# Performance work log

Hardware: AMD Instinct MI355X
Metric: run time of the kernel (lower is better)

The kernel has to match this reference:

```python
import jax, jax.numpy as jnp
import numpy as np

B, T, HID, H, DH, K = 2, 1024, 1024, 16, 64, 4
ROPE_BASE = 10000.0
EPS = 1e-6


def _causal_dwconv(x, w, b):
    # x: (B, T, C); w: (C, 1, K) depthwise; causal left-pad K-1, then SiLU
    xc = jnp.transpose(x, (0, 2, 1))  # (B, C, T)
    y = jax.lax.conv_general_dilated(
        xc, w, window_strides=(1,), padding=[(K - 1, 0)],
        dimension_numbers=('NCH', 'OIH', 'NCH'), feature_group_count=xc.shape[1])
    y = y + b[None, :, None]
    return jax.nn.silu(jnp.transpose(y, (0, 2, 1)))


def _rope(x, cos, sin):
    # x: (B, T, H, D); cos/sin: (T, D) with emb = cat(freqs, freqs)
    c = cos[None, :, None, :]
    s = sin[None, :, None, :]
    x1, x2 = x[..., ::2], x[..., 1::2]
    return jnp.concatenate(
        [x1 * c[..., ::2] - x2 * s[..., ::2],
         x1 * s[..., ::2] + x2 * c[..., ::2]], axis=-1)


def _delta_rule(q, k, v, alpha, beta, D_param):
    # q,k,v: (B,T,H,DH); alpha,beta: (B,T,H)
    # S_t = alpha_t * (I - beta_t k_t k_t^T) S_{t-1} + beta_t k_t v_t^T
    # o_t  = q_t^T S_t-1-style readout + D * (q.k) * v   (matches torch einsum 'bhd,bhde->bhe')
    qs = jnp.moveaxis(q, 1, 0).astype(jnp.float32)  # (T,B,H,DH)
    ks = jnp.moveaxis(k, 1, 0).astype(jnp.float32)
    vs = jnp.moveaxis(v, 1, 0).astype(jnp.float32)
    als = jnp.moveaxis(alpha, 1, 0).astype(jnp.float32)  # (T,B,H)
    bes = jnp.moveaxis(beta, 1, 0).astype(jnp.float32)

    def step(S, inp):
        qt, kt, vt, at, bt = inp
        ot = jnp.einsum('bhd,bhde->bhe', qt, S)
        ot = ot + D_param[None, :, None] * jnp.sum(qt * kt, -1, keepdims=True) * vt
        kS = jnp.einsum('bhd,bhde->bhe', kt, S)  # k^T S
        at_ = at[..., None, None]
        bt_ = bt[..., None, None]
        S_new = at_ * (S - bt_ * kt[..., :, None] * kS[..., None, :]) \
                + bt_ * kt[..., :, None] * vt[..., None, :]
        return S_new, ot

    S0 = jnp.zeros((q.shape[0], H, DH, DH), jnp.float32)
    _, outs = jax.lax.scan(step, S0, (qs, ks, vs, als, bes))
    return jnp.moveaxis(outs, 0, 1)  # (B,T,H,DH)


def _forward(x, Wq, Wk, Wv, Wg, Wo, bw, bb, gkw, gkb,
             qcw, qcb, kcw, kcb, vcw, vcb, A_log, D_param, dt_bias, onorm_w):
    Bb, Tt, _ = x.shape
    q = _causal_dwconv(x @ Wq, qcw, qcb).reshape(Bb, Tt, H, DH)
    k = _causal_dwconv(x @ Wk, kcw, kcb).reshape(Bb, Tt, H, DH)
    v = _causal_dwconv(x @ Wv, vcw, vcb).reshape(Bb, Tt, H, DH)

    # RoPE (computed on the fly, fp32)
    t = jnp.arange(Tt, dtype=jnp.float32)
    inv_freq = 1.0 / (ROPE_BASE ** (jnp.arange(0, DH, 2, dtype=jnp.float32) / DH))
    freqs = jnp.outer(t, inv_freq)
    emb = jnp.concatenate([freqs, freqs], -1)
    cos, sin = jnp.cos(emb), jnp.sin(emb)
    q = _rope(q, cos, sin)
    k = _rope(k, cos, sin)

    # L2-normalize q/k (delta-net stability, NOT softmax)
    q = q * jax.lax.rsqrt(jnp.sum(q * q, -1, keepdims=True) + EPS)
    k = k * jax.lax.rsqrt(jnp.sum(k * k, -1, keepdims=True) + EPS)

    beta = jax.nn.sigmoid(x @ bw + bb)  # (B,T,H) writing strength
    alpha = jnp.exp(-jnp.exp(A_log) * jax.nn.softplus(x @ gkw + gkb + dt_bias))  # (B,T,H) decay

    o = _delta_rule(q, k, v, alpha, beta, D_param)  # (B,T,H,DH)

    # gated RMSNorm output: g * silu(RMSNorm(o))
    g = (x @ Wg).reshape(Bb, Tt, H, DH)
    on = o * jax.lax.rsqrt(jnp.mean(o * o, -1, keepdims=True) + EPS) * onorm_w
    o = g * jax.nn.silu(on)
    return o.reshape(Bb, Tt, H * DH) @ Wo


def setup_inputs() -> dict:
    key = jax.random.key(0)
    ks = jax.random.split(key, 20)
    w = lambda i, shape, s=0.02: (jax.random.normal(ks[i], shape, jnp.float32) * s)
    return {
        'x': jax.random.normal(ks[0], (B, T, HID), jnp.float32),
        'Wq': w(1, (HID, H * DH)), 'Wk': w(2, (HID, H * DH)),
        'Wv': w(3, (HID, H * DH)), 'Wg': w(4, (HID, H * DH)),
        'Wo': w(5, (H * DH, HID)),
        'bw': w(6, (HID, H)), 'bb': jnp.zeros((H,), jnp.float32),
        'gkw': w(7, (HID, H)), 'gkb': jnp.zeros((H,), jnp.float32),
        'qcw': w(8, (H * DH, 1, K), 0.3), 'qcb': jnp.zeros((H * DH,), jnp.float32),
        'kcw': w(9, (H * DH, 1, K), 0.3), 'kcb': jnp.zeros((H * DH,), jnp.float32),
        'vcw': w(10, (H * DH, 1, K), 0.3), 'vcb': jnp.zeros((H * DH,), jnp.float32),
        'A_log': jnp.log(jax.random.uniform(ks[11], (H,), jnp.float32, 1.0, 16.0)),
        'D_param': jnp.ones((H,), jnp.float32),
        'dt_bias': jax.random.uniform(ks[12], (H,), jnp.float32, -0.01, 0.01),
        'onorm_w': jnp.ones((DH,), jnp.float32),
    }


def reference(x, Wq, Wk, Wv, Wg, Wo, bw, bb, gkw, gkb,
              qcw, qcb, kcw, kcb, vcw, vcb, A_log, D_param, dt_bias, onorm_w):
    return _forward(x, Wq, Wk, Wv, Wg, Wo, bw, bb, gkw, gkb,
                    qcw, qcb, kcw, kcb, vcw, vcb, A_log, D_param, dt_bias, onorm_w)
```

## Files before the change

### kernel.cpp

```cpp
#include <hip/hip_runtime.h>
#include <hip/hip_bf16.h>
#include <cstdint>

#define T_LEN 1024
#define HIDN  1024
#define NH    16
#define DHD   64

typedef __bf16 bf16x8 __attribute__((ext_vector_type(8)));
typedef float  f32x4  __attribute__((ext_vector_type(4)));

__device__ inline void split8(float4 x0, float4 x1, uint4& hi, uint4& lo) {
  union { __bf16 h[8]; uint4 u; } ph, pl;
  float v[8] = {x0.x, x0.y, x0.z, x0.w, x1.x, x1.y, x1.z, x1.w};
#pragma unroll
  for (int j = 0; j < 8; j++) {
    __bf16 h = (__bf16)v[j];
    ph.h[j] = h;
    pl.h[j] = (__bf16)(v[j] - (float)h);
  }
  hi = ph.u; lo = pl.u;
}

__global__ __launch_bounds__(256) void k_transp_split(
    const float* __restrict__ W0, const float* __restrict__ W1,
    const float* __restrict__ W2, const float* __restrict__ W3,
    const float* __restrict__ W4,
    __bf16* __restrict__ H0, __bf16* __restrict__ H1, __bf16* __restrict__ H2,
    __bf16* __restrict__ H3, __bf16* __restrict__ H4,
    __bf16* __restrict__ L0, __bf16* __restrict__ L1, __bf16* __restrict__ L2,
    __bf16* __restrict__ L3, __bf16* __restrict__ L4) {
  const float* W; __bf16* Th; __bf16* Tl;
  switch (blockIdx.z) {
    case 0: W = W0; Th = H0; Tl = L0; break;
    case 1: W = W1; Th = H1; Tl = L1; break;
    case 2: W = W2; Th = H2; Tl = L2; break;
    case 3: W = W3; Th = H3; Tl = L3; break;
    default: W = W4; Th = H4; Tl = L4; break;
  }
  __shared__ float tile[64][65];
  int tid = threadIdx.x;
  int r0 = tid >> 4;
  int c0 = (tid & 15) * 4;
  int kbase = blockIdx.y * 64, nbase = blockIdx.x * 64;
#pragma unroll
  for (int rr = 0; rr < 4; rr++) {
    int r = r0 + rr * 16;
    float4 v = *(const float4*)(W + (size_t)(kbase + r) * 1024 + nbase + c0);
    tile[r][c0 + 0] = v.x; tile[r][c0 + 1] = v.y;
    tile[r][c0 + 2] = v.z; tile[r][c0 + 3] = v.w;
  }
  __syncthreads();
#pragma unroll
  for (int rr = 0; rr < 4; rr++) {
    int n = r0 + rr * 16;
    union { __bf16 h[4]; unsigned long long u; } ph, pl;
#pragma unroll
    for (int j = 0; j < 4; j++) {
      float v = tile[c0 + j][n];
      __bf16 h = (__bf16)v;
      ph.h[j] = h;
      pl.h[j] = (__bf16)(v - (float)h);
    }
    *(unsigned long long*)(Th + (size_t)(nbase + n) * 1024 + kbase + c0) = ph.u;
    *(unsigned long long*)(Tl + (size_t)(nbase + n) * 1024 + kbase + c0) = pl.u;
  }
}

#define LDT 40
__global__ __launch_bounds__(256) void k_gemm3f(
    const float* __restrict__ Af,
    const __bf16* __restrict__ Bh0, const __bf16* __restrict__ Bh1,
    const __bf16* __restrict__ Bh2, const __bf16* __restrict__ Bh3,
    const __bf16* __restrict__ Bl0, const __bf16* __restrict__ Bl1,
    const __bf16* __restrict__ Bl2, const __bf16* __restrict__ Bl3,
    float* __restrict__ C0, float* __restrict__ C1,
    float* __restrict__ C2, float* __restrict__ C3,
    int Kdim, int Ncols) {
  const __bf16* Bh; const __bf16* Bl; float* C;
  switch (blockIdx.z) {
    case 0: Bh = Bh0; Bl = Bl0; C = C0; break;
    case 1: Bh = Bh1; Bl = Bl1; C = C1; break;
    case 2: Bh = Bh2; Bl = Bl2; C = C2; break;
    default: Bh = Bh3; Bl = Bl3; C = C3; break;
  }
  __shared__ __bf16 Ash[128 * LDT];
  __shared__ __bf16 Asl[128 * LDT];
  __shared__ __bf16 Bsh[128 * LDT];
  __shared__ __bf16 Bsl[128 * LDT];
  const int tid = threadIdx.x;
  const int lane = tid & 63;
  const int wave = tid >> 6;
  const int wr = wave >> 1, wc = wave & 1;
  const int rowA0 = blockIdx.y * 128;
  const int colB0 = blockIdx.x * 128;
  const int sseg = tid & 3;
  const int srow0 = tid >> 2;
  const int srow1 = srow0 + 64;

  f32x4 acc[4][4] = {};

  for (int k0 = 0; k0 < Kdim; k0 += 32) {
    size_t a0 = (size_t)(rowA0 + srow0) * Kdim + k0 + sseg * 8;
    size_t a1 = (size_t)(rowA0 + srow1) * Kdim + k0 + sseg * 8;
    size_t b0 = (size_t)(colB0 + srow0) * Kdim + k0 + sseg * 8;
    size_t b1 = (size_t)(colB0 + srow1) * Kdim + k0 + sseg * 8;
    float4 a00 = *(const float4*)(Af + a0);
    float4 a01 = *(const float4*)(Af + a0 + 4);
    float4 a10 = *(const float4*)(Af + a1);
    float4 a11 = *(const float4*)(Af + a1 + 4);
    uint4 rbh0 = *(const uint4*)(Bh + b0);
    uint4 rbh1 = *(const uint4*)(Bh + b1);
    uint4 rbl0 = *(const uint4*)(Bl + b0);
    uint4 rbl1 = *(const uint4*)(Bl + b1);
    uint4 rah0, ral0, rah1, ral1;
    split8(a00, a01, rah0, ral0);
    split8(a10, a11, rah1, ral1);
    __syncthreads();
    *(uint4*)&Ash[srow0 * LDT + sseg * 8] = rah0;
    *(uint4*)&Ash[srow1 * LDT + sseg * 8] = rah1;
    *(uint4*)&Asl[srow0 * LDT + sseg * 8] = ral0;
    *(uint4*)&Asl[srow1 * LDT + sseg * 8] = ral1;
    *(uint4*)&Bsh[srow0 * LDT + sseg * 8] = rbh0;
    *(uint4*)&Bsh[srow1 * LDT + sseg * 8] = rbh1;
    *(uint4*)&Bsl[srow0 * LDT + sseg * 8] = rbl0;
    *(uint4*)&Bsl[srow1 * LDT + sseg * 8] = rbl1;
    __syncthreads();
    bf16x8 afh[4], afl[4], bfh[4], bfl[4];
#pragma unroll
    for (int mi = 0; mi < 4; mi++) {
      int off = (wr * 64 + mi * 16 + (lane & 15)) * LDT + (lane >> 4) * 8;
      afh[mi] = *(const bf16x8*)&Ash[off];
      afl[mi] = *(const bf16x8*)&Asl[off];
    }
#pragma unroll
    for (int ni = 0; ni < 4; ni++) {
      int off = (wc * 64 + ni * 16 + (lane & 15)) * LDT + (lane >> 4) * 8;
      bfh[ni] = *(const bf16x8*)&Bsh[off];
      bfl[ni] = *(const bf16x8*)&Bsl[off];
    }
#pragma unroll
    for (int mi = 0; mi < 4; mi++)
#pragma unroll
      for (int ni = 0; ni < 4; ni++) {
        acc[mi][ni] = __builtin_amdgcn_mfma_f32_16x16x32_bf16(afh[mi], bfh[ni], acc[mi][ni], 0, 0, 0);
        acc[mi][ni] = __builtin_amdgcn_mfma_f32_16x16x32_bf16(afl[mi], bfh[ni], acc[mi][ni], 0, 0, 0);
        acc[mi][ni] = __builtin_amdgcn_mfma_f32_16x16x32_bf16(afh[mi], bfl[ni], acc[mi][ni], 0, 0, 0);
      }
  }
#pragma unroll
  for (int mi = 0; mi < 4; mi++)
#pragma unroll
    for (int ni = 0; ni < 4; ni++) {
      int col = colB0 + wc * 64 + ni * 16 + (lane & 15);
#pragma unroll
      for (int r = 0; r < 4; r++) {
        int row = rowA0 + wr * 64 + mi * 16 + (lane >> 4) * 4 + r;
        C[(size_t)row * Ncols + col] = acc[mi][ni][r];
      }
    }
}

__global__ __launch_bounds__(256) void k_gates(
    const float* __restrict__ x, const float* __restrict__ bw,
    const float* __restrict__ bb, const float* __restrict__ gkw,
    const float* __restrict__ gkb, const float* __restrict__ A_log,
    const float* __restrict__ dt_bias,
    float* __restrict__ alphaB, float* __restrict__ betaB) {
  const int bt = blockIdx.x;
  const int tid = threadIdx.x;
  const int h = tid & 15;
  const int chunk = tid >> 4;
  const float* xr = x + (size_t)bt * HIDN;
  float d1 = 0.f, d2 = 0.f;
#pragma unroll 8
  for (int j = 0; j < 64; j++) {
    int k = chunk * 64 + j;
    float xv = xr[k];
    d1 += xv * bw[k * 16 + h];
    d2 += xv * gkw[k * 16 + h];
  }
  __shared__ float p1[16][16], p2[16][16];
  p1[chunk][h] = d1; p2[chunk][h] = d2;
  __syncthreads();
  if (tid < 16) {
    float s1 = 0.f, s2 = 0.f;
#pragma unroll
    for (int c = 0; c < 16; c++) { s1 += p1[c][tid]; s2 += p2[c][tid]; }
    float beta = 1.f / (1.f + expf(-(s1 + bb[tid])));
    float z = s2 + gkb[tid] + dt_bias[tid];
    float sp = fmaxf(z, 0.f) + log1pf(expf(-fabsf(z)));
    float alpha = expf(-expf(A_log[tid]) * sp);
    alphaB[(size_t)bt * 16 + tid] = alpha;
    betaB[(size_t)bt * 16 + tid] = beta;
  }
}

__global__ __launch_bounds__(256) void k_cra(
    const float* __restrict__ qp, const float* __restrict__ kp,
    const float* __restrict__ vp,
    const float* __restrict__ qcw, const float* __restrict__ qcb,
    const float* __restrict__ kcw, const float* __restrict__ kcb,
    const float* __restrict__ vcw, const float* __restrict__ vcb,
    const float* __restrict__ alphaB, const float* __restrict__ betaB,
    const float* __restrict__ Dp,
    float* __restrict__ qr, float* __restrict__ kr, float* __restrict__ vr,
    float4* __restrict__ aux) {
  int widx = blockIdx.x * 4 + (threadIdx.x >> 6);
  int lane = threadIdx.x & 63;
  int h = widx & 15;
  int bt = widx >> 4;
  int t = bt & 1023, b = bt >> 10;
  int c = h * 64 + lane;
  size_t colbase = ((size_t)b * 1024) * 1024 + c;

  float4 wq = *(const float4*)(qcw + (size_t)c * 4);
  float4 wk = *(const float4*)(kcw + (size_t)c * 4);
  float4 wv = *(const float4*)(vcw + (size_t)c * 4);
  float aq = qcb[c], ak = kcb[c], av = vcb[c];
  {
    float x0 = qp[colbase + (size_t)t * 1024];
    float y0 = kp[colbase + (size_t)t * 1024];
    float z0 = vp[colbase + (size_t)t * 1024];
    aq += wq.w * x0; ak += wk.w * y0; av += wv.w * z0;
    if (t >= 1) {
      float x1 = qp[colbase + (size_t)(t - 1) * 1024];
      float y1 = kp[colbase + (size_t)(t - 1) * 1024];
      float z1 = vp[colbase + (size_t)(t - 1) * 1024];
      aq += wq.z * x1; ak += wk.z * y1; av += wv.z * z1;
    }
    if (t >= 2) {
      float x2 = qp[colbase + (size_t)(t - 2) * 1024];
      float y2 = kp[colbase + (size_t)(t - 2) * 1024];
      float z2v = vp[colbase + (size_t)(t - 2) * 1024];
      aq += wq.y * x2; ak += wk.y * y2; av += wv.y * z2v;
    }
    if (t >= 3) {
      float x3 = qp[colbase + (size_t)(t - 3) * 1024];
      float y3 = kp[colbase + (size_t)(t - 3) * 1024];
      float z3 = vp[colbase + (size_t)(t - 3) * 1024];
      aq += wq.x * x3; ak += wk.x * y3; av += wv.x * z3;
    }
  }
  float yq = aq / (1.f + expf(-aq));
  float yk = ak / (1.f + expf(-ak));
  float yv = av / (1.f + expf(-av));

  int i = lane & 31;
  float fr = expf(-(float)(2 * (i & 15)) * (9.210340371976184f / 32.f));
  float ang = (float)t * fr;
  float cv = cosf(ang), sv = sinf(ang);
  float q1 = __shfl(yq, 2 * i), q2 = __shfl(yq, 2 * i + 1);
  float k1 = __shfl(yk, 2 * i), k2 = __shfl(yk, 2 * i + 1);
  float qo = (lane < 32) ? (q1 * cv - q2 * sv) : (q1 * sv + q2 * cv);
  float ko = (lane < 32) ? (k1 * cv - k2 * sv) : (k1 * sv + k2 * cv);

  float qs = qo * qo, ks2 = ko * ko;
#pragma unroll
  for (int m = 1; m < 64; m <<= 1) { qs += __shfl_xor(qs, m); ks2 += __shfl_xor(ks2, m); }
  float qn = qo * rsqrtf(qs + 1e-6f);
  float kn = ko * rsqrtf(ks2 + 1e-6f);
  float dq = qn * kn;
#pragma unroll
  for (int m = 1; m < 64; m <<= 1) dq += __shfl_xor(dq, m);
  size_t obase = ((size_t)(b * 16 + h) * 1024 + t) * 64;
  qr[obase + lane] = qn;
  kr[obase + lane] = kn;
  vr[obase + lane] = yv;
  if (lane == 0) {
    float alpha = alphaB[(size_t)bt * 16 + h];
    float beta = betaB[(size_t)bt * 16 + h];
    aux[(size_t)(b * 16 + h) * 1024 + t] = make_float4(alpha, beta, alpha * beta, Dp[h] * dq);
  }
}

__global__ __launch_bounds__(256) void k_scanA(
    const float* __restrict__ qr, const float* __restrict__ kr,
    const float* __restrict__ vr, const float4* __restrict__ aux,
    float* __restrict__ O1, float* __restrict__ AcF,
    float* __restrict__ BcTF, float* __restrict__ QeffF,
    float* __restrict__ gcF) {
  const int bid = blockIdx.x;
  const int bh = bid >> 4, c = bid & 15;
  const int t0 = c * 64;
  const int tid = threadIdx.x;
  const int w = tid >> 6, lane = tid & 63;
  const float* qB = qr + (size_t)bh * 65536 + (size_t)t0 * 64;
  const float* kB = kr + (size_t)bh * 65536 + (size_t)t0 * 64;
  const float* vB = vr + (size_t)bh * 65536 + (size_t)t0 * 64;
  const float4* auxB = aux + (size_t)bh * T_LEN + t0;

  __shared__ __bf16 q_b[64 * 72];
  __shared__ __bf16 k_b[64 * 72];
  __shared__ __bf16 kT_b[64 * 72];
  __shared__ __bf16 C_b[64 * 72];
  __shared__ __bf16 U0T[64 * 72];
  __shared__ __bf16 WT[64 * 72];
  __shared__ float  vS[64 * 64];
  __shared__ float  MTf[64 * 68];
  __shared__ float  lgS[64], pvS[64], beS[64], awS[64], enS[64];

  if (w == 0) {
    float4 a4 = auxB[lane];
    float lg = logf(a4.x);
#pragma unroll
    for (int off = 1; off < 64; off <<= 1) {
      float tv = __shfl_up(lg, off);
      if (lane >= off) lg += tv;
    }
    float pv = __shfl_up(lg, 1);
    if (lane == 0) pv = 0.f;
    float lgTot = __shfl(lg, 63);
    lgS[lane] = lg; pvS[lane] = pv; beS[lane] = a4.y; awS[lane] = a4.w;
    enS[lane] = expf(lgTot - lg);
    if (lane == 0) gcF[bid] = expf(lgTot);
  }
#pragma unroll
  for (int p = 0; p < 2; p++) {
    int s = p * 256 + tid;
    int row = s >> 3, col8 = s & 7;
    const float* gq = qB + (size_t)row * 64 + col8 * 8;
    const float* gk = kB + (size_t)row * 64 + col8 * 8;
    const float* gv = vB + (size_t)row * 64 + col8 * 8;
    float4 q0 = *(const float4*)gq, q1 = *(const float4*)(gq + 4);
    float4 k0 = *(const float4*)gk, k1 = *(const float4*)(gk + 4);
    float4 v0 = *(const float4*)gv, v1 = *(const float4*)(gv + 4);
    union { __bf16 h[8]; uint4 u; } pq, pk;
    pq.h[0] = (__bf16)q0.x; pq.h[1] = (__bf16)q0.y; pq.h[2] = (__bf16)q0.z; pq.h[3] = (__bf16)q0.w;
    pq.h[4] = (__bf16)q1.x; pq.h[5] = (__bf16)q1.y; pq.h[6] = (__bf16)q1.z; pq.h[7] = (__bf16)q1.w;
    pk.h[0] = (__bf16)k0.x; pk.h[1] = (__bf16)k0.y; pk.h[2] = (__bf16)k0.z; pk.h[3] = (__bf16)k0.w;
    pk.h[4] = (__bf16)k1.x; pk.h[5] = (__bf16)k1.y; pk.h[6] = (__bf16)k1.z; pk.h[7] = (__bf16)k1.w;
    *(uint4*)&q_b[row * 72 + col8 * 8] = pq.u;
    *(uint4*)&k_b[row * 72 + col8 * 8] = pk.u;
    *(float4*)&vS[row * 64 + col8 * 8] = v0;
    *(float4*)&vS[row * 64 + col8 * 8 + 4] = v1;
  }
  __syncthreads();

  {
    const int mi = w;
#pragma unroll
    for (int ni = 0; ni < 4; ni++) {
      f32x4 akk = {0.f, 0.f, 0.f, 0.f};
      f32x4 aqk = {0.f, 0.f, 0.f, 0.f};
#pragma unroll
      for (int ks = 0; ks < 2; ks++) {
        bf16x8 fa_k = *(const bf16x8*)&k_b[(mi * 16 + (lane & 15)) * 72 + ks * 32 + (lane >> 4) * 8];
        bf16x8 fa_q = *(const bf16x8*)&q_b[(mi * 16 + (lane & 15)) * 72 + ks * 32 + (lane >> 4) * 8];
        bf16x8 fb_k = *(const bf16x8*)&k_b[(ni * 16 + (lane & 15)) * 72 + ks * 32 + (lane >> 4) * 8];
        akk = __builtin_amdgcn_mfma_f32_16x16x32_bf16(fa_k, fb_k, akk, 0, 0, 0);
        aqk = __builtin_amdgcn_mfma_f32_16x16x32_bf16(fa_q, fb_k, aqk, 0, 0, 0);
      }
#pragma unroll
      for (int r = 0; r < 4; r++) {
        int row = mi * 16 + (lane >> 4) * 4 + r;
        int col = ni * 16 + (lane & 15);
        float mt = 0.f, cv = 0.f;
        if (row > col) {
          mt = beS[row] * expf(lgS[row] - lgS[col]) * akk[r];
          cv = expf(pvS[row] - lgS[col]) * aqk[r];
        }
        MTf[col * 68 + row] = mt;
        C_b[row * 72 + col] = (__bf16)cv;
      }
    }
  }
  __syncthreads();

  if (w == 2) {
#pragma unroll
    for (int t8 = 0; t8 < 8; t8++) {
      union { __bf16 h[8]; uint4 u; } pt;
#pragma unroll
      for (int q = 0; q < 8; q++) {
        int t = t8 * 8 + q;
        pt.h[q] = (__bf16)((float)k_b[t * 72 + lane] * enS[t]);
      }
      *(uint4*)&kT_b[lane * 72 + t8 * 8] = pt.u;
    }
  }
  if (w < 2) {
    float u[64];
    if (w == 0) {
#pragma unroll
      for (int j = 0; j < 64; j++) u[j] = beS[j] * vS[j * 64 + lane];
    } else {
#pragma unroll
      for (int j = 0; j < 64; j++) u[j] = beS[j] * expf(lgS[j]) * (float)k_b[j * 72 + lane];
    }
    __bf16* dst = (w == 0) ? U0T : WT;
#pragma unroll
    for (int j = 0; j < 64; j++) {
      dst[lane * 72 + j] = (__bf16)u[j];
      float uj = u[j];
#pragma unroll
      for (int g = (j >> 4); g < 4; g++) {
#pragma unroll
        for (int q4 = 0; q4 < 4; q4++) {
          const float4 m4 = *(const float4*)&MTf[j * 68 + g * 16 + q4 * 4];
          u[g * 16 + q4 * 4 + 0] -= m4.x * uj;
          u[g * 16 + q4 * 4 + 1] -= m4.y * uj;
          u[g * 16 + q4 * 4 + 2] -= m4.z * uj;
          u[g * 16 + q4 * 4 + 3] -= m4.w * uj;
        }
      }
    }
  }
  __syncthreads();

  size_t cb = (size_t)bid * 4096;
  const int mi0 = (w >> 1) * 2;
  if ((w & 1) == 0) {
#pragma unroll
    for (int mm = 0; mm < 2; mm++) {
      int mi = mi0 + mm;
#pragma unroll
      for (int ni = 0; ni < 4; ni++) {
        f32x4 ab = {0.f, 0.f, 0.f, 0.f};
        f32x4 aa = {0.f, 0.f, 0.f, 0.f};
#pragma unroll
        for (int ks = 0; ks < 2; ks++) {
          int aoff = (mi * 16 + (lane & 15)) * 72 + ks * 32 + (lane >> 4) * 8;
          int boff = (ni * 16 + (lane & 15)) * 72 + ks * 32 + (lane >> 4) * 8;
          bf16x8 fu = *(const bf16x8*)&U0T[aoff];
          bf16x8 fkm = *(const bf16x8*)&kT_b[aoff];
          bf16x8 fkn = *(const bf16x8*)&kT_b[boff];
          bf16x8 fw = *(const bf16x8*)&WT[boff];
          ab = __builtin_amdgcn_mfma_f32_16x16x32_bf16(fu, fkn, ab, 0, 0, 0);
          aa = __builtin_amdgcn_mfma_f32_16x16x32_bf16(fkm, fw, aa, 0, 0, 0);
        }
#pragma unroll
        for (int r = 0; r < 4; r++) {
          int row = mi * 16 + (lane >> 4) * 4 + r;
          int col = ni * 16 + (lane & 15);
          BcTF[cb + row * 64 + col] = ab[r];
          AcF[cb + row * 64 + col] = aa[r];
        }
      }
    }
  } else {
#pragma unroll
    for (int mm = 0; mm < 2; mm++) {
      int mi = mi0 + mm;
#pragma unroll
      for (int ni = 0; ni < 4; ni++) {
        f32x4 ao = {0.f, 0.f, 0.f, 0.f};
        f32x4 ac = {0.f, 0.f, 0.f, 0.f};
#pragma unroll
        for (int ks = 0; ks < 2; ks++) {
          int aoff = (mi * 16 + (lane & 15)) * 72 + ks * 32 + (lane >> 4) * 8;
          int boff = (ni * 16 + (lane & 15)) * 72 + ks * 32 + (lane >> 4) * 8;
          bf16x8 fc = *(const bf16x8*)&C_b[aoff];
          bf16x8 fu = *(const bf16x8*)&U0T[boff];
          bf16x8 fw = *(const bf16x8*)&WT[boff];
          ao = __builtin_amdgcn_mfma_f32_16x16x32_bf16(fc, fu, ao, 0, 0, 0);
          ac = __builtin_amdgcn_mfma_f32_16x16x32_bf16(fc, fw, ac, 0, 0, 0);
        }
#pragma unroll
        for (int r = 0; r < 4; r++) {
          int t = mi * 16 + (lane >> 4) * 4 + r;
          int col = ni * 16 + (lane & 15);
          O1[(size_t)bh * 65536 + (size_t)(t0 + t) * 64 + col] =
              ao[r] + awS[t] * vS[t * 64 + col];
          QeffF[cb + t * 64 + col] = expf(pvS[t]) * (float)q_b[t * 72 + col] - ac[r];
        }
      }
    }
  }
}

__global__ __launch_bounds__(256) void k_scanB(
    const float* __restrict__ AcF, const float* __restrict__ BcTF,
    const float* __restrict__ gcF, float* __restrict__ S0TF) {
  const int bid = blockIdx.x;
  const int bh = bid >> 2, eg = bid & 3;
  const int e0 = eg * 16;
  const int tid = threadIdx.x;
  const int w = tid >> 6, lane = tid & 63;
  const int er = tid >> 2, seg = (tid & 3) * 16;
  const int er2 = tid >> 4, seg2 = (tid & 15) * 4;
  __shared__ float STf[16 * 68];
  __shared__ __bf16 Sh[16 * 72], Sl[16 * 72], Ac_b[64 * 72];
  *(float4*)&STf[er2 * 68 + seg2] = make_float4(0.f, 0.f, 0.f, 0.f);
  __syncthreads();

  size_t cbase = (size_t)bh * 16 * 4096;
  float4 acR[4];
  float bctR[4];
#pragma unroll
  for (int i = 0; i < 4; i++)
    acR[i] = *(const float4*)&AcF[cbase + er * 64 + seg + i * 4];
#pragma unroll
  for (int r = 0; r < 4; r++)
    bctR[r] = BcTF[cbase + (size_t)(e0 + (lane >> 4) * 4 + r) * 64 + w * 16 + (lane & 15)];

  for (int c = 0; c < 16; c++) {
    size_t cb = cbase + (size_t)c * 4096;
    {
      float4 s = *(const float4*)&STf[er2 * 68 + seg2];
      *(float4*)&S0TF[cb + (size_t)(e0 + er2) * 64 + seg2] = s;
      union { __bf16 h[4]; unsigned long long u; } ph, pl;
      float sv[4] = {s.x, s.y, s.z, s.w};
#pragma unroll
      for (int q = 0; q < 4; q++) {
        __bf16 hv = (__bf16)sv[q];
        ph.h[q] = hv;
        pl.h[q] = (__bf16)(sv[q] - (float)hv);
      }
      *(unsigned long long*)&Sh[er2 * 72 + seg2] = ph.u;
      *(unsigned long long*)&Sl[er2 * 72 + seg2] = pl.u;
    }
#pragma unroll
    for (int i = 0; i < 4; i++) {
      union { __bf16 h[4]; unsigned long long u; } pa;
      pa.h[0] = (__bf16)acR[i].x; pa.h[1] = (__bf16)acR[i].y;
      pa.h[2] = (__bf16)acR[i].z; pa.h[3] = (__bf16)acR[i].w;
      *(unsigned long long*)&Ac_b[er * 72 + seg + i * 4] = pa.u;
    }
    float gC = gcF[bh * 16 + c];
    __syncthreads();

    float4 acN[4];
    float bctN[4];
    if (c < 15) {
      size_t nb = cb + 4096;
#pragma unroll
      for (int i = 0; i < 4; i++)
        acN[i] = *(const float4*)&AcF[nb + er * 64 + seg + i * 4];
#pragma unroll
      for (int r = 0; r < 4; r++)
        bctN[r] = BcTF[nb + (size_t)(e0 + (lane >> 4) * 4 + r) * 64 + w * 16 + (lane & 15)];
    } else {
#pragma unroll
      for (int i = 0; i < 4; i++) acN[i] = acR[i];
#pragma unroll
      for (int r = 0; r < 4; r++) bctN[r] = bctR[r];
    }

    f32x4 acc = {0.f, 0.f, 0.f, 0.f};
#pragma unroll
    for (int ks = 0; ks < 2; ks++) {
      int aoff = (lane & 15) * 72 + ks * 32 + (lane >> 4) * 8;
      int boff = (w * 16 + (lane & 15)) * 72 + ks * 32 + (lane >> 4) * 8;
      bf16x8 ah = *(const bf16x8*)&Sh[aoff];
      bf16x8 al = *(const bf16x8*)&Sl[aoff];
      bf16x8 bb = *(const bf16x8*)&Ac_b[boff];
      acc = __builtin_amdgcn_mfma_f32_16x16x32_bf16(ah, bb, acc, 0, 0, 0);
      acc = __builtin_amdgcn_mfma_f32_16x16x32_bf16(al, bb, acc, 0, 0, 0);
    }
#pragma unroll
    for (int r = 0; r < 4; r++) {
      int e = (lane >> 4) * 4 + r;
      int d = w * 16 + (lane & 15);
      STf[e * 68 + d] = gC * STf[e * 68 + d] - acc[r] + bctR[r];
    }
    __syncthreads();
#pragma unroll
    for (int i = 0; i < 4; i++) acR[i] = acN[i];
#pragma unroll
    for (int r = 0; r < 4; r++) bctR[r] = bctN[r];
  }
}

__global__ __launch_bounds__(256) void k_scanCn(
    const float* __restrict__ S0TF, const float* __restrict__ QeffF,
    const float* __restrict__ obuf, const float* __restrict__ g,
    const float* __restrict__ onw, float* __restrict__ robuf) {
  const int bid = blockIdx.x;
  const int bh = bid >> 4, c = bid & 15, t0c = c * 64;
  const int b = bh >> 4, h = bh & 15;
  const int tid = threadIdx.x;
  const int w = tid >> 6, lane = tid & 63;
  const int er = tid >> 2, seg = (tid & 3) * 16;
  size_t cb = (size_t)bid * 4096;
  __shared__ __bf16 Sh[64 * 72], Sl[64 * 72], Qb[64 * 72];
#pragma unroll
  for (int i = 0; i < 4; i++) {
    float4 s = *(const float4*)&S0TF[cb + er * 64 + seg + i * 4];
    union { __bf16 h[4]; unsigned long long u; } ph, pl;
    float sv[4] = {s.x, s.y, s.z, s.w};
#pragma unroll
    for (int q = 0; q < 4; q++) {
      __bf16 hv = (__bf16)sv[q];
      ph.h[q] = hv;
      pl.h[q] = (__bf16)(sv[q] - (float)hv);
    }
    *(unsigned long long*)&Sh[er * 72 + seg + i * 4] = ph.u;
    *(unsigned long long*)&Sl[er * 72 + seg + i * 4] = pl.u;
    float4 qq = *(const float4*)&QeffF[cb + er * 64 + seg + i * 4];
    union { __bf16 h[4]; unsigned long long u; } pq;
    pq.h[0] = (__bf16)qq.x; pq.h[1] = (__bf16)qq.y;
    pq.h[2] = (__bf16)qq.z; pq.h[3] = (__bf16)qq.w;
    *(unsigned long long*)&Qb[er * 72 + seg + i * 4] = pq.u;
  }
  __syncthreads();
  f32x4 acc[4];
#pragma unroll
  for (int ni = 0; ni < 4; ni++) {
    acc[ni] = (f32x4){0.f, 0.f, 0.f, 0.f};
#pragma unroll
    for (int ks = 0; ks < 2; ks++) {
      int aoff = (w * 16 + (lane & 15)) * 72 + ks * 32 + (lane >> 4) * 8;
      int boff = (ni * 16 + (lane & 15)) * 72 + ks * 32 + (lane >> 4) * 8;
      bf16x8 fq = *(const bf16x8*)&Qb[aoff];
      bf16x8 sh = *(const bf16x8*)&Sh[boff];
      bf16x8 sl = *(const bf16x8*)&Sl[boff];
      acc[ni] = __builtin_amdgcn_mfma_f32_16x16x32_bf16(fq, sh, acc[ni], 0, 0, 0);
      acc[ni] = __builtin_amdgcn_mfma_f32_16x16x32_bf16(fq, sl, acc[ni], 0, 0, 0);
    }
  }
  float onwv[4];
#pragma unroll
  for (int ni = 0; ni < 4; ni++) onwv[ni] = onw[ni * 16 + (lane & 15)];
#pragma unroll
  for (int r = 0; r < 4; r++) {
    int t = w * 16 + (lane >> 4) * 4 + r;
    float o[4];
#pragma unroll
    for (int ni = 0; ni < 4; ni++) {
      int e = ni * 16 + (lane & 15);
      o[ni] = obuf[(size_t)bh * 65536 + (size_t)(t0c + t) * 64 + e] + acc[ni][r];
    }
    float ss = o[0] * o[0] + o[1] * o[1] + o[2] * o[2] + o[3] * o[3];
    ss += __shfl_xor(ss, 1);
    ss += __shfl_xor(ss, 2);
    ss += __shfl_xor(ss, 4);
    ss += __shfl_xor(ss, 8);
    float rinv = rsqrtf(ss * (1.f / 64.f) + 1e-6f);
    size_t gbase = ((size_t)(b * 1024 + t0c + t)) * 1024 + h * 64;
#pragma unroll
    for (int ni = 0; ni < 4; ni++) {
      int e = ni * 16 + (lane & 15);
      float on = o[ni] * rinv * onwv[ni];
      float sil = on / (1.f + expf(-on));
      robuf[gbase + e] = g[gbase + e] * sil;
    }
  }
}

extern "C" void kernel_launch(void* const* d_in, const int* in_sizes, int n_in,
                              void* d_out, int out_size, void* d_ws, size_t ws_size,
                              hipStream_t stream) {
  (void)in_sizes; (void)n_in; (void)out_size; (void)ws_size;
  const float* x    = (const float*)d_in[0];
  const float* Wq   = (const float*)d_in[1];
  const float* Wk   = (const float*)d_in[2];
  const float* Wv   = (const float*)d_in[3];
  const float* Wg   = (const float*)d_in[4];
  const float* Wo   = (const float*)d_in[5];
  const float* bw   = (const float*)d_in[6];
  const float* bb   = (const float*)d_in[7];
  const float* gkw  = (const float*)d_in[8];
  const float* gkb  = (const float*)d_in[9];
  const float* qcw  = (const float*)d_in[10];
  const float* qcb  = (const float*)d_in[11];
  const float* kcw  = (const float*)d_in[12];
  const float* kcb  = (const float*)d_in[13];
  const float* vcw  = (const float*)d_in[14];
  const float* vcb  = (const float*)d_in[15];
  const float* A_log= (const float*)d_in[16];
  const float* Dp   = (const float*)d_in[17];
  const float* dtb  = (const float*)d_in[18];
  const float* onw  = (const float*)d_in[19];

  char* ws = (char*)d_ws;
  const size_t MB = 1024 * 1024;
  __bf16* Wq_h = (__bf16*)(ws + 8 * MB);
  __bf16* Wq_l = (__bf16*)(ws + 10 * MB);
  __bf16* Wk_h = (__bf16*)(ws + 12 * MB);
  __bf16* Wk_l = (__bf16*)(ws + 14 * MB);
  __bf16* Wv_h = (__bf16*)(ws + 16 * MB);
  __bf16* Wv_l = (__bf16*)(ws + 18 * MB);
  __bf16* Wg_h = (__bf16*)(ws + 20 * MB);
  __bf16* Wg_l = (__bf16*)(ws + 22 * MB);
  __bf16* Wo_h = (__bf16*)(ws + 24 * MB);
  __bf16* Wo_l = (__bf16*)(ws + 26 * MB);
  float* q_pre = (float*)(ws + 28 * MB);
  float* k_pre = (float*)(ws + 36 * MB);
  float* v_pre = (float*)(ws + 44 * MB);
  float* g_buf = (float*)(ws + 52 * MB);
  float* qrb   = (float*)(ws + 0);
  float* krb   = (float*)(ws + 8 * MB);
  float* vr    = (float*)(ws + 16 * MB);
  float* obuf  = v_pre;
  float* AcF   = (float*)(ws + 28 * MB);
  float* BcTF  = (float*)(ws + 36 * MB);
  float* S0TF  = (float*)(ws + 0);
  float* QeffF = (float*)(ws + 16 * MB);
  float* robuf = (float*)(ws + 8 * MB);
  float* alphaB = (float*)(ws + 60 * MB);
  float* betaB  = (float*)(ws + 60 * MB + 128 * 1024);
  float4* aux   = (float4*)(ws + 60 * MB + 256 * 1024);
  float* gcF    = (float*)(ws + 60 * MB + 768 * 1024);
  float* out    = (float*)d_out;

  k_transp_split<<<dim3(16, 16, 5), 256, 0, stream>>>(
      Wq, Wk, Wv, Wg, Wo,
      Wq_h, Wk_h, Wv_h, Wg_h, Wo_h,
      Wq_l, Wk_l, Wv_l, Wg_l, Wo_l);
  k_gates<<<2048, 256, 0, stream>>>(x, bw, bb, gkw, gkb, A_log, dtb, alphaB, betaB);
  k_gemm3f<<<dim3(8, 16, 4), 256, 0, stream>>>(
      x,
      Wq_h, Wk_h, Wv_h, Wg_h,
      Wq_l, Wk_l, Wv_l, Wg_l,
      q_pre, k_pre, v_pre, g_buf, 1024, 1024);
  k_cra<<<8192, 256, 0, stream>>>(q_pre, k_pre, v_pre,
                                  qcw, qcb, kcw, kcb, vcw, vcb,
                                  alphaB, betaB, Dp, qrb, krb, vr, aux);
  k_scanA<<<512, 256, 0, stream>>>(qrb, krb, vr, aux, obuf, AcF, BcTF, QeffF, gcF);
  k_scanB<<<128, 256, 0, stream>>>(AcF, BcTF, gcF, S0TF);
  k_scanCn<<<512, 256, 0, stream>>>(S0TF, QeffF, obuf, g_buf, onw, robuf);
  k_gemm3f<<<dim3(8, 16, 1), 256, 0, stream>>>(
      robuf,
      Wo_h, Wo_h, Wo_h, Wo_h,
      Wo_l, Wo_l, Wo_l, Wo_l,
      out, out, out, out, 1024, 1024);
}
```

Before: 320.9 us.

## Fuse conv/RoPE/norm prologue into chunk scan kernel and store Ac/Qeff as bf16

The separate k_cra kernel (causal depthwise conv, SiLU, RoPE, L2 norm, q·k dot) is folded into k_scanA. Each warp computes 16 timesteps of its chunk directly from the pre-projection buffers into shared memory, using a sliding register window for the conv taps. This removes one kernel launch and the fp32 qr/kr/vr/aux round trip through global memory. The Ac and Qeff intermediates are also written in bf16 rather than fp32, halving their traffic in scanB and scanCn, which previously converted them to bf16 anyway. The fused prologue runs sequential per-warp work with many shuffle reductions inside scanA, which launches only 512 blocks.

```diff
diff --git a/kernel.cpp b/kernel.cpp
--- a/kernel.cpp
+++ b/kernel.cpp
@@ -196,7 +196,7 @@
   }
 }
 
-__global__ __launch_bounds__(256) void k_cra(
+__global__ __launch_bounds__(256) void k_scanA(
     const float* __restrict__ qp, const float* __restrict__ kp,
     const float* __restrict__ vp,
     const float* __restrict__ qcw, const float* __restrict__ qcb,
@@ -204,91 +204,15 @@
     const float* __restrict__ vcw, const float* __restrict__ vcb,
     const float* __restrict__ alphaB, const float* __restrict__ betaB,
     const float* __restrict__ Dp,
-    float* __restrict__ qr, float* __restrict__ kr, float* __restrict__ vr,
-    float4* __restrict__ aux) {
-  int widx = blockIdx.x * 4 + (threadIdx.x >> 6);
-  int lane = threadIdx.x & 63;
-  int h = widx & 15;
-  int bt = widx >> 4;
-  int t = bt & 1023, b = bt >> 10;
-  int c = h * 64 + lane;
-  size_t colbase = ((size_t)b * 1024) * 1024 + c;
-
-  float4 wq = *(const float4*)(qcw + (size_t)c * 4);
-  float4 wk = *(const float4*)(kcw + (size_t)c * 4);
-  float4 wv = *(const float4*)(vcw + (size_t)c * 4);
-  float aq = qcb[c], ak = kcb[c], av = vcb[c];
-  {
-    float x0 = qp[colbase + (size_t)t * 1024];
-    float y0 = kp[colbase + (size_t)t * 1024];
-    float z0 = vp[colbase + (size_t)t * 1024];
-    aq += wq.w * x0; ak += wk.w * y0; av += wv.w * z0;
-    if (t >= 1) {
-      float x1 = qp[colbase + (size_t)(t - 1) * 1024];
-      float y1 = kp[colbase + (size_t)(t - 1) * 1024];
-      float z1 = vp[colbase + (size_t)(t - 1) * 1024];
-      aq += wq.z * x1; ak += wk.z * y1; av += wv.z * z1;
-    }
-    if (t >= 2) {
-      float x2 = qp[colbase + (size_t)(t - 2) * 1024];
-      float y2 = kp[colbase + (size_t)(t - 2) * 1024];
-      float z2v = vp[colbase + (size_t)(t - 2) * 1024];
-      aq += wq.y * x2; ak += wk.y * y2; av += wv.y * z2v;
-    }
-    if (t >= 3) {
-      float x3 = qp[colbase + (size_t)(t - 3) * 1024];
-      float y3 = kp[colbase + (size_t)(t - 3) * 1024];
-      float z3 = vp[colbase + (size_t)(t - 3) * 1024];
-      aq += wq.x * x3; ak += wk.x * y3; av += wv.x * z3;
-    }
-  }
-  float yq = aq / (1.f + expf(-aq));
-  float yk = ak / (1.f + expf(-ak));
-  float yv = av / (1.f + expf(-av));
-
-  int i = lane & 31;
-  float fr = expf(-(float)(2 * (i & 15)) * (9.210340371976184f / 32.f));
-  float ang = (float)t * fr;
-  float cv = cosf(ang), sv = sinf(ang);
-  float q1 = __shfl(yq, 2 * i), q2 = __shfl(yq, 2 * i + 1);
-  float k1 = __shfl(yk, 2 * i), k2 = __shfl(yk, 2 * i + 1);
-  float qo = (lane < 32) ? (q1 * cv - q2 * sv) : (q1 * sv + q2 * cv);
-  float ko = (lane < 32) ? (k1 * cv - k2 * sv) : (k1 * sv + k2 * cv);
-
-  float qs = qo * qo, ks2 = ko * ko;
-#pragma unroll
-  for (int m = 1; m < 64; m <<= 1) { qs += __shfl_xor(qs, m); ks2 += __shfl_xor(ks2, m); }
-  float qn = qo * rsqrtf(qs + 1e-6f);
-  float kn = ko * rsqrtf(ks2 + 1e-6f);
-  float dq = qn * kn;
-#pragma unroll
-  for (int m = 1; m < 64; m <<= 1) dq += __shfl_xor(dq, m);
-  size_t obase = ((size_t)(b * 16 + h) * 1024 + t) * 64;
-  qr[obase + lane] = qn;
-  kr[obase + lane] = kn;
-  vr[obase + lane] = yv;
-  if (lane == 0) {
-    float alpha = alphaB[(size_t)bt * 16 + h];
-    float beta = betaB[(size_t)bt * 16 + h];
-    aux[(size_t)(b * 16 + h) * 1024 + t] = make_float4(alpha, beta, alpha * beta, Dp[h] * dq);
-  }
-}
-
-__global__ __launch_bounds__(256) void k_scanA(
-    const float* __restrict__ qr, const float* __restrict__ kr,
-    const float* __restrict__ vr, const float4* __restrict__ aux,
-    float* __restrict__ O1, float* __restrict__ AcF,
-    float* __restrict__ BcTF, float* __restrict__ QeffF,
+    float* __restrict__ O1, __bf16* __restrict__ AcB,
+    float* __restrict__ BcTF, __bf16* __restrict__ QeffB,
     float* __restrict__ gcF) {
   const int bid = blockIdx.x;
   const int bh = bid >> 4, c = bid & 15;
+  const int b = bh >> 4, h = bh & 15;
   const int t0 = c * 64;
   const int tid = threadIdx.x;
   const int w = tid >> 6, lane = tid & 63;
-  const float* qB = qr + (size_t)bh * 65536 + (size_t)t0 * 64;
-  const float* kB = kr + (size_t)bh * 65536 + (size_t)t0 * 64;
-  const float* vB = vr + (size_t)bh * 65536 + (size_t)t0 * 64;
-  const float4* auxB = aux + (size_t)bh * T_LEN + t0;
 
   __shared__ __bf16 q_b[64 * 72];
   __shared__ __bf16 k_b[64 * 72];
@@ -300,9 +224,70 @@
   __shared__ float  MTf[64 * 68];
   __shared__ float  lgS[64], pvS[64], beS[64], awS[64], enS[64];
 
+  {
+    const int cch = h * 64 + lane;
+    const size_t bbase = ((size_t)b << 20) + cch;
+    const float* qpb = qp + bbase;
+    const float* kpb = kp + bbase;
+    const float* vpb = vp + bbase;
+    float4 wq = *(const float4*)(qcw + (size_t)cch * 4);
+    float4 wk = *(const float4*)(kcw + (size_t)cch * 4);
+    float4 wv = *(const float4*)(vcw + (size_t)cch * 4);
+    const float bq = qcb[cch], bk = kcb[cch], bv = vcb[cch];
+    const float Dh = Dp[h];
+    const int tstart = t0 + w * 16;
+    float xq3 = (tstart >= 3) ? qpb[(size_t)(tstart - 3) * 1024] : 0.f;
+    float xq2 = (tstart >= 2) ? qpb[(size_t)(tstart - 2) * 1024] : 0.f;
+    float xq1 = (tstart >= 1) ? qpb[(size_t)(tstart - 1) * 1024] : 0.f;
+    float xk3 = (tstart >= 3) ? kpb[(size_t)(tstart - 3) * 1024] : 0.f;
+    float xk2 = (tstart >= 2) ? kpb[(size_t)(tstart - 2) * 1024] : 0.f;
+    float xk1 = (tstart >= 1) ? kpb[(size_t)(tstart - 1) * 1024] : 0.f;
+    float xv3 = (tstart >= 3) ? vpb[(size_t)(tstart - 3) * 1024] : 0.f;
+    float xv2 = (tstart >= 2) ? vpb[(size_t)(tstart - 2) * 1024] : 0.f;
+    float xv1 = (tstart >= 1) ? vpb[(size_t)(tstart - 1) * 1024] : 0.f;
+    const int i = lane & 31;
+    const float fr = expf(-(float)(2 * (i & 15)) * (9.210340371976184f / 32.f));
+#pragma unroll
+    for (int ii = 0; ii < 16; ii++) {
+      const int tg = tstart + ii;
+      float xq0 = qpb[(size_t)tg * 1024];
+      float xk0 = kpb[(size_t)tg * 1024];
+      float xv0 = vpb[(size_t)tg * 1024];
+      float aq = bq + wq.x * xq3 + wq.y * xq2 + wq.z * xq1 + wq.w * xq0;
+      float ak = bk + wk.x * xk3 + wk.y * xk2 + wk.z * xk1 + wk.w * xk0;
+      float av = bv + wv.x * xv3 + wv.y * xv2 + wv.z * xv1 + wv.w * xv0;
+      float yq = aq / (1.f + expf(-aq));
+      float yk = ak / (1.f + expf(-ak));
+      float yv = av / (1.f + expf(-av));
+      float ang = (float)tg * fr;
+      float cv = cosf(ang), sv = sinf(ang);
+      float q1 = __shfl(yq, 2 * i), q2 = __shfl(yq, 2 * i + 1);
+      float k1 = __shfl(yk, 2 * i), k2 = __shfl(yk, 2 * i + 1);
+      float qo = (lane < 32) ? (q1 * cv - q2 * sv) : (q1 * sv + q2 * cv);
+      float ko = (lane < 32) ? (k1 * cv - k2 * sv) : (k1 * sv + k2 * cv);
+      float qs = qo * qo, ks2 = ko * ko;
+#pragma unroll
+      for (int m = 1; m < 64; m <<= 1) { qs += __shfl_xor(qs, m); ks2 += __shfl_xor(ks2, m); }
+      float qn = qo * rsqrtf(qs + 1e-6f);
+      float kn = ko * rsqrtf(ks2 + 1e-6f);
+      float dq = qn * kn;
+#pragma unroll
+      for (int m = 1; m < 64; m <<= 1) dq += __shfl_xor(dq, m);
+      const int tl = w * 16 + ii;
+      q_b[tl * 72 + lane] = (__bf16)qn;
+      k_b[tl * 72 + lane] = (__bf16)kn;
+      vS[tl * 64 + lane] = yv;
+      if (lane == 0) awS[tl] = Dh * dq;
+      xq3 = xq2; xq2 = xq1; xq1 = xq0;
+      xk3 = xk2; xk2 = xk1; xk1 = xk0;
+      xv3 = xv2; xv2 = xv1; xv1 = xv0;
+    }
+  }
   if (w == 0) {
-    float4 a4 = auxB[lane];
-    float lg = logf(a4.x);
+    size_t gi = (size_t)(b * 1024 + t0 + lane) * 16 + h;
+    float alpha = alphaB[gi];
+    float beta = betaB[gi];
+    float lg = logf(alpha);
 #pragma unroll
     for (int off = 1; off < 64; off <<= 1) {
       float tv = __shfl_up(lg, off);
@@ -311,29 +296,9 @@
     float pv = __shfl_up(lg, 1);
     if (lane == 0) pv = 0.f;
     float lgTot = __shfl(lg, 63);
-    lgS[lane] = lg; pvS[lane] = pv; beS[lane] = a4.y; awS[lane] = a4.w;
+    lgS[lane] = lg; pvS[lane] = pv; beS[lane] = beta;
     enS[lane] = expf(lgTot - lg);
     if (lane == 0) gcF[bid] = expf(lgTot);
-  }
-#pragma unroll
-  for (int p = 0; p < 2; p++) {
-    int s = p * 256 + tid;
-    int row = s >> 3, col8 = s & 7;
-    const float* gq = qB + (size_t)row * 64 + col8 * 8;
-    const float* gk = kB + (size_t)row * 64 + col8 * 8;
-    const float* gv = vB + (size_t)row * 64 + col8 * 8;
-    float4 q0 = *(const float4*)gq, q1 = *(const float4*)(gq + 4);
-    float4 k0 = *(const float4*)gk, k1 = *(const float4*)(gk + 4);
-    float4 v0 = *(const float4*)gv, v1 = *(const float4*)(gv + 4);
-    union { __bf16 h[8]; uint4 u; } pq, pk;
-    pq.h[0] = (__bf16)q0.x; pq.h[1] = (__bf16)q0.y; pq.h[2] = (__bf16)q0.z; pq.h[3] = (__bf16)q0.w;
-    pq.h[4] = (__bf16)q1.x; pq.h[5] = (__bf16)q1.y; pq.h[6] = (__bf16)q1.z; pq.h[7] = (__bf16)q1.w;
-    pk.h[0] = (__bf16)k0.x; pk.h[1] = (__bf16)k0.y; pk.h[2] = (__bf16)k0.z; pk.h[3] = (__bf16)k0.w;
-    pk.h[4] = (__bf16)k1.x; pk.h[5] = (__bf16)k1.y; pk.h[6] = (__bf16)k1.z; pk.h[7] = (__bf16)k1.w;
-    *(uint4*)&q_b[row * 72 + col8 * 8] = pq.u;
-    *(uint4*)&k_b[row * 72 + col8 * 8] = pk.u;
-    *(float4*)&vS[row * 64 + col8 * 8] = v0;
-    *(float4*)&vS[row * 64 + col8 * 8 + 4] = v1;
   }
   __syncthreads();
 
@@ -434,7 +399,7 @@
           int row = mi * 16 + (lane >> 4) * 4 + r;
           int col = ni * 16 + (lane & 15);
           BcTF[cb + row * 64 + col] = ab[r];
-          AcF[cb + row * 64 + col] = aa[r];
+          AcB[cb + row * 64 + col] = (__bf16)aa[r];
         }
       }
     }
@@ -462,7 +427,8 @@
           int col = ni * 16 + (lane & 15);
           O1[(size_t)bh * 65536 + (size_t)(t0 + t) * 64 + col] =
               ao[r] + awS[t] * vS[t * 64 + col];
-          QeffF[cb + t * 64 + col] = expf(pvS[t]) * (float)q_b[t * 72 + col] - ac[r];
+          QeffB[cb + t * 64 + col] =
+              (__bf16)(expf(pvS[t]) * (float)q_b[t * 72 + col] - ac[r]);
         }
       }
     }
@@ -470,7 +436,7 @@
 }
 
 __global__ __launch_bounds__(256) void k_scanB(
-    const float* __restrict__ AcF, const float* __restrict__ BcTF,
+    const __bf16* __restrict__ AcB, const float* __restrict__ BcTF,
     const float* __restrict__ gcF, float* __restrict__ S0TF) {
   const int bid = blockIdx.x;
   const int bh = bid >> 2, eg = bid & 3;
@@ -485,11 +451,10 @@
   __syncthreads();
 
   size_t cbase = (size_t)bh * 16 * 4096;
-  float4 acR[4];
+  uint4 acR0, acR1;
   float bctR[4];
-#pragma unroll
-  for (int i = 0; i < 4; i++)
-    acR[i] = *(const float4*)&AcF[cbase + er * 64 + seg + i * 4];
+  acR0 = *(const uint4*)&AcB[cbase + er * 64 + seg];
+  acR1 = *(const uint4*)&AcB[cbase + er * 64 + seg + 8];
 #pragma unroll
   for (int r = 0; r < 4; r++)
     bctR[r] = BcTF[cbase + (size_t)(e0 + (lane >> 4) * 4 + r) * 64 + w * 16 + (lane & 15)];
@@ -510,29 +475,21 @@
       *(unsigned long long*)&Sh[er2 * 72 + seg2] = ph.u;
       *(unsigned long long*)&Sl[er2 * 72 + seg2] = pl.u;
     }
-#pragma unroll
-    for (int i = 0; i < 4; i++) {
-      union { __bf16 h[4]; unsigned long long u; } pa;
-      pa.h[0] = (__bf16)acR[i].x; pa.h[1] = (__bf16)acR[i].y;
-      pa.h[2] = (__bf16)acR[i].z; pa.h[3] = (__bf16)acR[i].w;
-      *(unsigned long long*)&Ac_b[er * 72 + seg + i * 4] = pa.u;
-    }
+    *(uint4*)&Ac_b[er * 72 + seg] = acR0;
+    *(uint4*)&Ac_b[er * 72 + seg + 8] = acR1;
     float gC = gcF[bh * 16 + c];
     __syncthreads();
 
-    float4 acN[4];
+    uint4 acN0 = acR0, acN1 = acR1;
     float bctN[4];
     if (c < 15) {
       size_t nb = cb + 4096;
-#pragma unroll
-      for (int i = 0; i < 4; i++)
-        acN[i] = *(const float4*)&AcF[nb + er * 64 + seg + i * 4];
+      acN0 = *(const uint4*)&AcB[nb + er * 64 + seg];
+      acN1 = *(const uint4*)&AcB[nb + er * 64 + seg + 8];
 #pragma unroll
       for (int r = 0; r < 4; r++)
         bctN[r] = BcTF[nb + (size_t)(e0 + (lane >> 4) * 4 + r) * 64 + w * 16 + (lane & 15)];
     } else {
-#pragma unroll
-      for (int i = 0; i < 4; i++) acN[i] = acR[i];
 #pragma unroll
       for (int r = 0; r < 4; r++) bctN[r] = bctR[r];
     }
@@ -555,15 +512,14 @@
       STf[e * 68 + d] = gC * STf[e * 68 + d] - acc[r] + bctR[r];
     }
     __syncthreads();
-#pragma unroll
-    for (int i = 0; i < 4; i++) acR[i] = acN[i];
+    acR0 = acN0; acR1 = acN1;
 #pragma unroll
     for (int r = 0; r < 4; r++) bctR[r] = bctN[r];
   }
 }
 
 __global__ __launch_bounds__(256) void k_scanCn(
-    const float* __restrict__ S0TF, const float* __restrict__ QeffF,
+    const float* __restrict__ S0TF, const __bf16* __restrict__ QeffB,
     const float* __restrict__ obuf, const float* __restrict__ g,
     const float* __restrict__ onw, float* __restrict__ robuf) {
   const int bid = blockIdx.x;
@@ -587,11 +543,12 @@
     }
     *(unsigned long long*)&Sh[er * 72 + seg + i * 4] = ph.u;
     *(unsigned long long*)&Sl[er * 72 + seg + i * 4] = pl.u;
-    float4 qq = *(const float4*)&QeffF[cb + er * 64 + seg + i * 4];
-    union { __bf16 h[4]; unsigned long long u; } pq;
-    pq.h[0] = (__bf16)qq.x; pq.h[1] = (__bf16)qq.y;
-    pq.h[2] = (__bf16)qq.z; pq.h[3] = (__bf16)qq.w;
-    *(unsigned long long*)&Qb[er * 72 + seg + i * 4] = pq.u;
+  }
+  {
+    uint4 qv0 = *(const uint4*)&QeffB[cb + er * 64 + seg];
+    uint4 qv1 = *(const uint4*)&QeffB[cb + er * 64 + seg + 8];
+    *(uint4*)&Qb[er * 72 + seg] = qv0;
+    *(uint4*)&Qb[er * 72 + seg + 8] = qv1;
   }
   __syncthreads();
   f32x4 acc[4];
@@ -679,19 +636,15 @@
   float* k_pre = (float*)(ws + 36 * MB);
   float* v_pre = (float*)(ws + 44 * MB);
   float* g_buf = (float*)(ws + 52 * MB);
-  float* qrb   = (float*)(ws + 0);
-  float* krb   = (float*)(ws + 8 * MB);
-  float* vr    = (float*)(ws + 16 * MB);
-  float* obuf  = v_pre;
-  float* AcF   = (float*)(ws + 28 * MB);
-  float* BcTF  = (float*)(ws + 36 * MB);
-  float* S0TF  = (float*)(ws + 0);
-  float* QeffF = (float*)(ws + 16 * MB);
-  float* robuf = (float*)(ws + 8 * MB);
+  float* obuf  = (float*)(ws + 0);
+  float* BcTF  = (float*)(ws + 8 * MB);
+  __bf16* QeffB = (__bf16*)(ws + 16 * MB);
+  __bf16* AcB   = (__bf16*)(ws + 20 * MB);
+  float* S0TF  = (float*)(ws + 28 * MB);
+  float* robuf = (float*)(ws + 36 * MB);
   float* alphaB = (float*)(ws + 60 * MB);
   float* betaB  = (float*)(ws + 60 * MB + 128 * 1024);
-  float4* aux   = (float4*)(ws + 60 * MB + 256 * 1024);
-  float* gcF    = (float*)(ws + 60 * MB + 768 * 1024);
+  float* gcF    = (float*)(ws + 60 * MB + 256 * 1024);
   float* out    = (float*)d_out;
 
   k_transp_split<<<dim3(16, 16, 5), 256, 0, stream>>>(
@@ -704,12 +657,12 @@
       Wq_h, Wk_h, Wv_h, Wg_h,
       Wq_l, Wk_l, Wv_l, Wg_l,
       q_pre, k_pre, v_pre, g_buf, 1024, 1024);
-  k_cra<<<8192, 256, 0, stream>>>(q_pre, k_pre, v_pre,
-                                  qcw, qcb, kcw, kcb, vcw, vcb,
-                                  alphaB, betaB, Dp, qrb, krb, vr, aux);
-  k_scanA<<<512, 256, 0, stream>>>(qrb, krb, vr, aux, obuf, AcF, BcTF, QeffF, gcF);
-  k_scanB<<<128, 256, 0, stream>>>(AcF, BcTF, gcF, S0TF);
-  k_scanCn<<<512, 256, 0, stream>>>(S0TF, QeffF, obuf, g_buf, onw, robuf);
+  k_scanA<<<512, 256, 0, stream>>>(q_pre, k_pre, v_pre,
+                                   qcw, qcb, kcw, kcb, vcw, vcb,
+                                   alphaB, betaB, Dp,
+                                   obuf, AcB, BcTF, QeffB, gcF);
+  k_scanB<<<128, 256, 0, stream>>>(AcB, BcTF, gcF, S0TF);
+  k_scanCn<<<512, 256, 0, stream>>>(S0TF, QeffB, obuf, g_buf, onw, robuf);
   k_gemm3f<<<dim3(8, 16, 1), 256, 0, stream>>>(
       robuf,
       Wo_h, Wo_h, Wo_h, Wo_h,
```

Result: no change. 320.9 us (-0.0%).
